# Optimization experiments

Hardware: AMD Instinct MI355X
Metric: run time of the kernel (lower is better)

## Reference

```python
import jax, jax.numpy as jnp
import numpy as np

N_NODES = 50000
N_EDGES = 800000
D_IN, D_HID, D_OUT = 16, 64, 16
N_BLOCKS = 4


def setup_inputs() -> dict:
    key = jax.random.key(0)
    ks = jax.random.split(key, 12)
    s = 0.05  # small init scale to keep sum-aggregation over 4 blocks stable
    return {
        "x": jax.random.normal(ks[0], (N_NODES, D_IN), jnp.float32),
        "lframes": jax.random.normal(ks[1], (N_NODES, 4, 4), jnp.float32),
        "edge_index": jax.random.randint(ks[2], (2, N_EDGES), 0, N_NODES, jnp.int64),
        "lin_in_w": jax.random.normal(ks[3], (D_IN, D_HID), jnp.float32) * s,
        "lin_in_b": jnp.zeros((D_HID,), jnp.float32),
        # per-block mlp1: Linear(2D->D), ReLU, Linear(D->D), ReLU, Linear(D->D)
        "w0": jax.random.normal(ks[4], (N_BLOCKS, 2 * D_HID, D_HID), jnp.float32) * s,
        "b0": jnp.zeros((N_BLOCKS, D_HID), jnp.float32),
        "w1": jax.random.normal(ks[5], (N_BLOCKS, D_HID, D_HID), jnp.float32) * s,
        "b1": jnp.zeros((N_BLOCKS, D_HID), jnp.float32),
        "w2": jax.random.normal(ks[6], (N_BLOCKS, D_HID, D_HID), jnp.float32) * s,
        "b2": jnp.zeros((N_BLOCKS, D_HID), jnp.float32),
        "lin_out_w": jax.random.normal(ks[7], (D_HID, D_OUT), jnp.float32) * s,
        "lin_out_b": jnp.zeros((D_OUT,), jnp.float32),
    }


def reference(x, lframes, edge_index, lin_in_w, lin_in_b,
              w0, b0, w1, b1, w2, b2, lin_out_w, lin_out_b):
    src = edge_index[0]  # x_j (source / neighbor)
    dst = edge_index[1]  # x_i (target / aggregation node)
    h = x @ lin_in_w + lin_in_b  # [N, D]
    for k in range(N_BLOCKS):
        # message: cat((x_j, x_i)) -> mlp1 ; mlp2 is Identity (num_layers_mlp2=0)
        m = jnp.concatenate((h[src], h[dst]), axis=-1)  # [E, 2D]
        m = jax.nn.relu(m @ w0[k] + b0[k])
        m = jax.nn.relu(m @ w1[k] + b1[k])
        m = m @ w2[k] + b2[k]  # [E, D]
        # aggregate: scatter-add at target node
        h = jax.ops.segment_sum(m, dst, num_segments=N_NODES)
    return h @ lin_out_w + lin_out_b  # [N, D_OUT]
```

## Files before the change

kernel.cpp:

```cpp
#include <hip/hip_runtime.h>
#include <hip/hip_bf16.h>

#define N_NODES 50000
#define N_EDGES 800000
#define D_IN    16
#define D_HID   64
#define D_OUT   16
#define NCHUNK  ((N_NODES + 255) / 256)
#define TMAX    100352
#define GE4     ((N_EDGES / 4 + 255) / 256)
#define GH      ((N_NODES * D_HID + 255) / 256)
#define SCAP    48
#define NSLOT4  (N_NODES * SCAP / 4)

typedef __hip_bfloat16 bf16;
typedef _Float16 f16;
typedef _Float16 f16x8 __attribute__((ext_vector_type(8)));
typedef float    f32x4 __attribute__((ext_vector_type(4)));
typedef _Float16 f16x8a __attribute__((ext_vector_type(8), may_alias));
typedef int      i32x4 __attribute__((ext_vector_type(4)));
typedef unsigned short u16x8a __attribute__((ext_vector_type(8), may_alias));
typedef float    f32x4a __attribute__((ext_vector_type(4), may_alias));

__device__ __forceinline__ float b2f(bf16 v) { return __bfloat162float(v); }
__device__ __forceinline__ float bfb(unsigned short u) {
    union { unsigned u; float f; } z; z.u = (unsigned)u << 16; return z.f;
}
__device__ __forceinline__ int clampn(int v) {
    return v < 0 ? 0 : (v >= N_NODES ? N_NODES - 1 : v);
}
__device__ __forceinline__ float rdf(const void* p, long i, int isbf) {
    return isbf ? b2f(((const bf16*)p)[i]) : ((const float*)p)[i];
}
__device__ __forceinline__ f16x8 relu8(f16x8 v) {
#pragma unroll
    for (int j = 0; j < 8; j++) v[j] = v[j] > (f16)0 ? v[j] : (f16)0;
    return v;
}
__device__ __forceinline__ int sbase(int m) {
    return (m & 0xFFFFF) * SCAP + ((m >> 25) & 3) * 16;
}

__global__ __launch_bounds__(256) void k_detect(const unsigned short* __restrict__ xw,
                                                const int* __restrict__ ei,
                                                int* __restrict__ flags,
                                                int* __restrict__ cursor,
                                                int* __restrict__ slots,
                                                unsigned short* __restrict__ psrc_us)
{
    int gtid = blockIdx.x * 256 + threadIdx.x;
    if (gtid < N_NODES) cursor[gtid] = 0;
    const i32x4 fillv = {N_NODES, N_NODES, N_NODES, N_NODES};
#pragma unroll
    for (int k = 0; k < 12; k++) {
        int q = k * (NCHUNK * 256) + gtid;
        if (q < NSLOT4) ((i32x4*)slots)[q] = fillv;
    }
    if (blockIdx.x == 0 && threadIdx.x < 64)
        psrc_us[(size_t)N_NODES * 64 + threadIdx.x] = 0xFC00u;
    if (blockIdx.x == 0 && threadIdx.x == 0) {
        int inband = 0;
        for (int j = 0; j < 256; j++) {
            unsigned short w = xw[2 * j];
            int e = (w >> 7) & 0xFF;
            if ((w & 0x7FFF) == 0 || (e >= 100 && e <= 140)) inband++;
        }
        flags[0] = (inband >= 192) ? 1 : 0;
        int z = 1;
        for (int j = 1; j < 128; j += 2) z &= (ei[j] == 0) ? 1 : 0;
        flags[1] = z;
    }
}

__global__ __launch_bounds__(256) void k_scatter4(const int* __restrict__ flags,
                                                  const int* __restrict__ eidx,
                                                  int* __restrict__ cursor,
                                                  int* __restrict__ slots)
{
    int base = (blockIdx.x * 256 + threadIdx.x) * 4;
    if (base >= N_EDGES) return;
    const int strd = flags[1] ? 2 : 1;
    const long dbase = flags[1] ? (long)(2 * N_EDGES) : (long)N_EDGES;
    int d[4], s[4], pos[4], cnt = min(4, N_EDGES - base);
#pragma unroll
    for (int j = 0; j < 4; j++)
        if (j < cnt) {
            d[j] = clampn(eidx[dbase + (long)(base + j) * strd]);
            s[j] = clampn(eidx[(long)(base + j) * strd]);
        }
#pragma unroll
    for (int j = 0; j < 4; j++)
        if (j < cnt) pos[j] = atomicAdd(&cursor[d[j]], 1);
#pragma unroll
    for (int j = 0; j < 4; j++)
        if (j < cnt && pos[j] < SCAP) slots[d[j] * SCAP + pos[j]] = s[j];
}

__global__ __launch_bounds__(256) void k_prep(const int* __restrict__ flags,
                                              const void* __restrict__ gw0,
                                              const void* __restrict__ gw1,
                                              const void* __restrict__ gw2,
                                              f16* __restrict__ wfrag,
                                              const void* __restrict__ x,
                                              const void* __restrict__ liw,
                                              const void* __restrict__ lib,
                                              float* __restrict__ h,
                                              const void* __restrict__ gb1,
                                              const void* __restrict__ gb2,
                                              float* __restrict__ cpad)
{
    const int isbf = flags[0];
    const int bid = blockIdx.x;
    if (bid < 32) {
        int idx = bid * 256 + threadIdx.x;
        int kb = idx >> 11, rem = idx & 2047;
        int slot = rem >> 6, lane = rem & 63;
        int lm = lane & 15, quad = lane >> 4;
        f16* outp = wfrag + (long)idx * 8;
        if (slot < 16) {
            int c = slot >> 2, q = slot & 3;
            long base = (long)kb * 2 * D_HID * D_HID;
#pragma unroll
            for (int j = 0; j < 8; j++)
                outp[j] = (f16)rdf(gw0, base + (long)(c * 32 + quad * 8 + j) * 64 + q * 16 + lm, isbf);
        } else {
            const void* gw = (slot < 24) ? gw1 : gw2;
            int s = (slot < 24) ? slot - 16 : slot - 24;
            int c = s >> 2, q = s & 3;
            long base = (long)kb * D_HID * D_HID;
#pragma unroll
            for (int j = 0; j < 8; j++)
                outp[j] = (f16)rdf(gw, base + (long)(c * 32 + quad * 8 + j) * 64 + q * 16 + lm, isbf);
        }
    } else if (bid < 32 + GH) {
        int idx = (bid - 32) * 256 + threadIdx.x;
        if (idx >= N_NODES * D_HID) return;
        int n = idx >> 6, c = idx & 63;
        float acc, wr[16], xr[16];
        if (isbf) {
            const unsigned short* xp = (const unsigned short*)x + (long)n * 16;
            u16x8a x0 = *(const u16x8a*)xp, x1 = *(const u16x8a*)(xp + 8);
#pragma unroll
            for (int i = 0; i < 8; i++) { xr[i] = bfb(x0[i]); xr[8 + i] = bfb(x1[i]); }
            const unsigned short* wq = (const unsigned short*)liw;
#pragma unroll
            for (int i = 0; i < 16; i++) wr[i] = bfb(wq[i * 64 + c]);
            acc = bfb(((const unsigned short*)lib)[c]);
        } else {
            const float* xp = (const float*)x + (long)n * 16;
#pragma unroll
            for (int q = 0; q < 4; q++) {
                f32x4a v = *(const f32x4a*)(xp + q * 4);
#pragma unroll
                for (int j = 0; j < 4; j++) xr[q * 4 + j] = v[j];
            }
            const float* wq = (const float*)liw;
#pragma unroll
            for (int i = 0; i < 16; i++) wr[i] = wq[i * 64 + c];
            acc = ((const float*)lib)[c];
        }
#pragma unroll
        for (int i = 0; i < 16; i++) acc += xr[i] * wr[i];
        h[idx] = acc;
    } else {
        int t = threadIdx.x;
        int k = t >> 6, j = t & 63;
        float acc = rdf(gb2, (long)k * 64 + j, isbf);
        for (int i = 0; i < 64; i++) {
            float zi = (float)(f16)fmaxf(rdf(gb1, (long)k * 64 + i, isbf), 0.f);
            float wi = (float)(f16)rdf(gw2, (long)k * 4096 + (long)i * 64 + j, isbf);
            acc += zi * wi;
        }
        cpad[k * 64 + j] = acc;
    }
}

__global__ __launch_bounds__(256) void k_scan1(const int* __restrict__ deg,
                                               int* __restrict__ bsum_t)
{
    __shared__ int rt[256];
    const int t = threadIdx.x;
    int i = blockIdx.x * 256 + t;
    int v = (i < N_NODES) ? deg[i] : 0;
    rt[t] = min((v + 15) >> 4, 3);
    __syncthreads();
    for (int d = 128; d > 0; d >>= 1) {
        if (t < d) rt[t] += rt[t + d];
        __syncthreads();
    }
    if (t == 0) bsum_t[blockIdx.x] = rt[0];
}

__global__ __launch_bounds__(256) void k_scan2(const int* __restrict__ bsum_t,
                                               int* __restrict__ boff_t,
                                               int* __restrict__ tot_t)
{
    __shared__ int st_[256];
    const int t = threadIdx.x;
    st_[t] = (t < NCHUNK) ? bsum_t[t] : 0;
    __syncthreads();
    for (int d = 1; d < 256; d <<= 1) {
        int vt = (t >= d) ? st_[t - d] : 0;
        __syncthreads();
        st_[t] += vt;
        __syncthreads();
    }
    if (t < NCHUNK) boff_t[t] = (t == 0) ? 0 : st_[t - 1];
    if (t == NCHUNK - 1) tot_t[0] = st_[t];
}

__global__ __launch_bounds__(256) void k_scan3(const int* __restrict__ deg,
                                               const int* __restrict__ boff_t,
                                               int* __restrict__ toff,
                                               int* __restrict__ tmeta)
{
    __shared__ int st_[256];
    const int t = threadIdx.x;
    int i = blockIdx.x * 256 + t;
    int v = (i < N_NODES) ? deg[i] : 0;
    int w = min((v + 15) >> 4, 3);
    st_[t] = w;
    __syncthreads();
    for (int d = 1; d < 256; d <<= 1) {
        int ut = (t >= d) ? st_[t - d] : 0;
        __syncthreads();
        st_[t] += ut;
        __syncthreads();
    }
    if (i < N_NODES) {
        int exT = boff_t[blockIdx.x] + st_[t] - w;
        toff[i] = exT;
        for (int j = 0; j < w; j++)
            tmeta[exT + j] = i | (min(16, v - 16 * j) << 20) | (j << 25);
    }
}

#define HP_ST 72

__global__ __launch_bounds__(256) void k_proj(
    const int* __restrict__ flags, float* hio,
    const f16* __restrict__ wfrag, const void* __restrict__ gb0,
    const int* __restrict__ deg,
    f16* __restrict__ psrc, f16* __restrict__ pdst, int kblk)
{
    __shared__ f16 hL_s[4][16 * HP_ST];

    const int tid  = threadIdx.x;
    const int isbf = flags[0];
    const int wv = tid >> 6, ln = tid & 63;
    const int lm = ln & 15, quad = ln >> 4;
    f16* hL = hL_s[wv];

    const int g = blockIdx.x * 4 + wv;
    if (g >= N_NODES / 16) return;
    const int n0 = g * 16;

    const f16* wb = wfrag + (long)kblk * 32 * 64 * 8;

#pragma unroll
    for (int i = 0; i < 16; i++) {
        int idx = i * 64 + ln;
        hL[(idx >> 6) * HP_ST + (idx & 63)] = (f16)hio[(long)n0 * 64 + idx];
    }
#pragma unroll
    for (int i = 0; i < 16; i++)
        if (deg[n0 + i] == 0) hio[(long)(n0 + i) * 64 + ln] = 0.f;

    f16x8 a[2];
#pragma unroll
    for (int c = 0; c < 2; c++)
        a[c] = *(const f16x8a*)&hL[lm * HP_ST + c * 32 + quad * 8];

    f32x4 accS[4], accD[4];
#pragma unroll
    for (int q = 0; q < 4; q++) {
        float bd = rdf(gb0, (long)kblk * 64 + q * 16 + lm, isbf);
        accS[q] = (f32x4){0.f, 0.f, 0.f, 0.f};
        accD[q] = (f32x4){bd, bd, bd, bd};
    }
#pragma unroll
    for (int c = 0; c < 2; c++)
#pragma unroll
        for (int q = 0; q < 4; q++) {
            f16x8 bs = *(const f16x8a*)&wb[(((c + 0) * 4 + q) * 64 + ln) * 8];
            f16x8 bd = *(const f16x8a*)&wb[(((c + 2) * 4 + q) * 64 + ln) * 8];
            accS[q] = __builtin_amdgcn_mfma_f32_16x16x32_f16(a[c], bs, accS[q], 0, 0, 0);
            accD[q] = __builtin_amdgcn_mfma_f32_16x16x32_f16(a[c], bd, accD[q], 0, 0, 0);
        }
#pragma unroll
    for (int q = 0; q < 4; q++)
#pragma unroll
        for (int r = 0; r < 4; r++) {
            long o = (long)(n0 + quad * 4 + r) * 64 + q * 16 + lm;
            psrc[o] = (f16)accS[q][r];
            pdst[o] = (f16)accD[q][r];
        }
}

#define Y_ST 72

__global__ __launch_bounds__(256) void k_edge_tile(
    const int* __restrict__ flags,
    const int* __restrict__ slots, const int* __restrict__ tmeta,
    const int* __restrict__ toff,
    const f16* __restrict__ psrc, const f16* __restrict__ pdst,
    float* __restrict__ hout,
    const f16* __restrict__ wfrag, const void* __restrict__ gb1,
    const void* __restrict__ gb2, const float* __restrict__ cpad, int kblk)
{
    __shared__ f16 y_s[4][16 * Y_ST];

    const int tid  = threadIdx.x;
    const int isbf = flags[0];
    const int wv = tid >> 6, ln = tid & 63;
    const int lm = ln & 15, quad = ln >> 4;
    const int sub = ln & 7, eh = ln >> 3;
    f16* y = y_s[wv];

    const f16* wb = wfrag + (long)kblk * 32 * 64 * 8;
    f16x8 bw1[2][4], bw2[2][4];
#pragma unroll
    for (int c = 0; c < 2; c++)
#pragma unroll
        for (int q = 0; q < 4; q++) {
            bw1[c][q] = *(const f16x8a*)&wb[((16 + c * 4 + q) * 64 + ln) * 8];
            bw2[c][q] = *(const f16x8a*)&wb[((24 + c * 4 + q) * 64 + ln) * 8];
        }
    float bias1[4], bias2[4], cp[4];
#pragma unroll
    for (int q = 0; q < 4; q++) {
        bias1[q] = rdf(gb1, (long)kblk * 64 + q * 16 + lm, isbf);
        bias2[q] = rdf(gb2, (long)kblk * 64 + q * 16 + lm, isbf);
        cp[q]    = cpad[kblk * 64 + q * 16 + lm];
    }

    const int T  = toff[N_NODES];
    const int W  = gridDim.x * 4;
    const int gw = blockIdx.x * 4 + wv;
    int t0 = (int)((long)gw * T / W);
    int t1 = (int)((long)(gw + 1) * T / W);
    if (t0 > 0)
        while (t0 < T && (tmeta[t0] & 0xFFFFF) == (tmeta[t0 - 1] & 0xFFFFF)) t0++;
    if (t1 > 0)
        while (t1 < T && (tmeta[t1] & 0xFFFFF) == (tmeta[t1 - 1] & 0xFFFFF)) t1++;
    if (t0 >= t1) return;

    int mA = tmeta[t0];
    int mB = tmeta[min(t0 + 1, T - 1)];
    int mC = tmeta[min(t0 + 2, T - 1)];
    int bA = sbase(mA), bB = sbase(mB);
    int sAa = slots[bA + eh], sAb = slots[bA + 8 + eh];
    int sBa = slots[bB + eh], sBb = slots[bB + 8 + eh];
    f16x8 psAa = *(const f16x8a*)&psrc[(long)sAa * 64 + sub * 8];
    f16x8 psAb = *(const f16x8a*)&psrc[(long)sAb * 64 + sub * 8];
    f16x8 pdA  = *(const f16x8a*)&pdst[(long)(mA & 0xFFFFF) * 64 + sub * 8];

    float accn[4] = {0.f, 0.f, 0.f, 0.f};

    for (int tt = t0; tt < t1; ++tt) {
        const int mD = tmeta[min(tt + 3, T - 1)];
        const int bC = sbase(mC);
        const int sCa = slots[bC + eh], sCb = slots[bC + 8 + eh];
        f16x8 psBa = *(const f16x8a*)&psrc[(long)sBa * 64 + sub * 8];
        f16x8 psBb = *(const f16x8a*)&psrc[(long)sBb * 64 + sub * 8];
        f16x8 pdB  = *(const f16x8a*)&pdst[(long)(mB & 0xFFFFF) * 64 + sub * 8];

        *(f16x8a*)&y[eh * Y_ST + sub * 8]       = relu8(psAa + pdA);
        *(f16x8a*)&y[(8 + eh) * Y_ST + sub * 8] = relu8(psAb + pdA);

        f16x8 a1[2];
        a1[0] = *(const f16x8a*)&y[lm * Y_ST + quad * 8];
        a1[1] = *(const f16x8a*)&y[lm * Y_ST + 32 + quad * 8];
        f32x4 acc[4];
#pragma unroll
        for (int q = 0; q < 4; q++)
            acc[q] = (f32x4){bias1[q], bias1[q], bias1[q], bias1[q]};
#pragma unroll
        for (int c = 0; c < 2; c++)
#pragma unroll
            for (int q = 0; q < 4; q++)
                acc[q] = __builtin_amdgcn_mfma_f32_16x16x32_f16(a1[c], bw1[c][q], acc[q], 0, 0, 0);
#pragma unroll
        for (int q = 0; q < 4; q++)
#pragma unroll
            for (int r = 0; r < 4; r++)
                y[(quad * 4 + r) * Y_ST + q * 16 + lm] = (f16)fmaxf(acc[q][r], 0.f);

        f16x8 a2[2];
        a2[0] = *(const f16x8a*)&y[lm * Y_ST + quad * 8];
        a2[1] = *(const f16x8a*)&y[lm * Y_ST + 32 + quad * 8];
#pragma unroll
        for (int q = 0; q < 4; q++)
            acc[q] = (f32x4){bias2[q], bias2[q], bias2[q], bias2[q]};
#pragma unroll
        for (int c = 0; c < 2; c++)
#pragma unroll
            for (int q = 0; q < 4; q++)
                acc[q] = __builtin_amdgcn_mfma_f32_16x16x32_f16(a2[c], bw2[c][q], acc[q], 0, 0, 0);

#pragma unroll
        for (int q = 0; q < 4; q++)
#pragma unroll
            for (int r = 0; r < 4; r++)
                accn[q] += acc[q][r];

        const int curn = mA & 0xFFFFF;
        const int nxt  = (tt + 1 < t1) ? (mB & 0xFFFFF) : -1;
        if (nxt != curn) {
            const float npad = (float)(16 - ((mA >> 20) & 31));
#pragma unroll
            for (int q = 0; q < 4; q++) {
                float v = accn[q];
                v += __shfl_xor(v, 16, 64);
                v += __shfl_xor(v, 32, 64);
                if (quad == 0) hout[(long)curn * 64 + q * 16 + lm] = v - npad * cp[q];
                accn[q] = 0.f;
            }
        }

        mA = mB; mB = mC; mC = mD;
        sBa = sCa; sBb = sCb;
        psAa = psBa; psAb = psBb; pdA = pdB;
    }
}

__global__ __launch_bounds__(256) void k_lin_out(const int* __restrict__ flags,
                                                 const float* __restrict__ h,
                                                 const void* __restrict__ w,
                                                 const void* __restrict__ b,
                                                 float* __restrict__ out)
{
    int idx = blockIdx.x * 256 + threadIdx.x;
    if (idx >= N_NODES * D_OUT) return;
    const int isbf = flags[0];
    int n = idx >> 4, c = idx & 15;
    float acc = rdf(b, c, isbf);
    const float* hr = h + (long)n * D_HID;
#pragma unroll
    for (int i = 0; i < D_HID; i++) acc += hr[i] * rdf(w, (long)i * D_OUT + c, isbf);
    out[idx] = acc;
}

extern "C" void kernel_launch(void* const* d_in, const int* in_sizes, int n_in,
                              void* d_out, int out_size, void* d_ws, size_t ws_size,
                              hipStream_t stream)
{
    const void* x    = d_in[0];
    const int*  ei   = (const int*)d_in[2];
    const void* liw  = d_in[3];
    const void* lib  = d_in[4];
    const void* w0   = d_in[5];
    const void* b0   = d_in[6];
    const void* w1   = d_in[7];
    const void* b1   = d_in[8];
    const void* w2   = d_in[9];
    const void* b2   = d_in[10];
    const void* low  = d_in[11];
    const void* lob  = d_in[12];
    float* out = (float*)d_out;

    char* wp = (char*)d_ws;
    int*   flags  = (int*)wp;                 wp += 256;
    float* hA     = (float*)wp;               wp += (size_t)N_NODES * D_HID * 4;
    f16*   Psrc   = (f16*)wp;                 wp += ((size_t)N_NODES + 1) * D_HID * 2;
    f16*   Pdst   = (f16*)wp;                 wp += (size_t)N_NODES * D_HID * 2;
    f16*   wfrag  = (f16*)wp;                 wp += (size_t)4 * 32 * 64 * 8 * 2;
    float* cpad   = (float*)wp;               wp += (size_t)4 * 64 * 4;
    int*   cursor = (int*)wp;                 wp += (size_t)N_NODES * 4;
    int*   bsum_t = (int*)wp;                 wp += 256 * 4;
    int*   boff_t = (int*)wp;                 wp += 256 * 4;
    int*   tmeta  = (int*)wp;                 wp += (size_t)TMAX * 4;
    int*   slots  = (int*)wp;                 wp += (size_t)N_NODES * SCAP * 4;
    int*   toff   = (int*)wp;

    k_detect<<<NCHUNK, 256, 0, stream>>>((const unsigned short*)x, ei, flags,
                                         cursor, slots, (unsigned short*)Psrc);
    k_scatter4<<<GE4, 256, 0, stream>>>(flags, ei, cursor, slots);
    k_prep<<<32 + GH + 1, 256, 0, stream>>>(flags, w0, w1, w2, wfrag,
                                            x, liw, lib, hA, b1, b2, cpad);

    k_scan1<<<NCHUNK, 256, 0, stream>>>(cursor, bsum_t);
    k_scan2<<<1, 256, 0, stream>>>(bsum_t, boff_t, toff + N_NODES);
    k_scan3<<<NCHUNK, 256, 0, stream>>>(cursor, boff_t, toff, tmeta);

    for (int k = 0; k < 4; k++) {
        k_proj<<<(N_NODES / 16 + 3) / 4, 256, 0, stream>>>(flags, hA, wfrag, b0,
                                                           cursor, Psrc, Pdst, k);
        k_edge_tile<<<1024, 256, 0, stream>>>(flags, slots, tmeta, toff,
                                              Psrc, Pdst, hA, wfrag, b1, b2,
                                              cpad, k);
    }

    k_lin_out<<<(N_NODES * D_OUT + 255) / 256, 256, 0, stream>>>(flags, hA, low, lob, out);
}
```

Baseline: 435.2 us.

## Store neighbor slots as 16-bit indices, widen scatter, cache lin_out weights in LDS

Shrinks the per-node neighbor slot array from 32-bit to 16-bit source indices, which halves slot fill and read traffic. The fill pattern becomes 0xC350 (50000) in each half-word. The scatter kernel now handles 8 edges per thread, k_lin_out stages weights and bias in shared memory and reads h with vector loads, and the edge tile kernel launches twice as many blocks. 16-bit indices only work because N_NODES fits in an unsigned short; the hidden edge kernel code must read slots as u16 correctly.

```diff
diff --git a/kernel.cpp b/kernel.cpp
--- a/kernel.cpp
+++ b/kernel.cpp
@@ -8,10 +8,10 @@
 #define D_OUT   16
 #define NCHUNK  ((N_NODES + 255) / 256)
 #define TMAX    100352
-#define GE4     ((N_EDGES / 4 + 255) / 256)
+#define GE8     ((N_EDGES / 8 + 255) / 256)
 #define GH      ((N_NODES * D_HID + 255) / 256)
 #define SCAP    48
-#define NSLOT4  (N_NODES * SCAP / 4)
+#define NSLOTV  (N_NODES * SCAP / 8)
 
 typedef __hip_bfloat16 bf16;
 typedef _Float16 f16;
@@ -45,16 +45,17 @@
                                                 const int* __restrict__ ei,
                                                 int* __restrict__ flags,
                                                 int* __restrict__ cursor,
-                                                int* __restrict__ slots,
+                                                unsigned short* __restrict__ slots,
                                                 unsigned short* __restrict__ psrc_us)
 {
     int gtid = blockIdx.x * 256 + threadIdx.x;
     if (gtid < N_NODES) cursor[gtid] = 0;
-    const i32x4 fillv = {N_NODES, N_NODES, N_NODES, N_NODES};
-#pragma unroll
-    for (int k = 0; k < 12; k++) {
+    const int dpat = (int)0xC350C350;
+    const i32x4 fillv = {dpat, dpat, dpat, dpat};
+#pragma unroll
+    for (int k = 0; k < 6; k++) {
         int q = k * (NCHUNK * 256) + gtid;
-        if (q < NSLOT4) ((i32x4*)slots)[q] = fillv;
+        if (q < NSLOTV) ((i32x4*)slots)[q] = fillv;
     }
     if (blockIdx.x == 0 && threadIdx.x < 64)
         psrc_us[(size_t)N_NODES * 64 + threadIdx.x] = 0xFC00u;
@@ -72,28 +73,29 @@
     }
 }
 
-__global__ __launch_bounds__(256) void k_scatter4(const int* __restrict__ flags,
+__global__ __launch_bounds__(256) void k_scatter8(const int* __restrict__ flags,
                                                   const int* __restrict__ eidx,
                                                   int* __restrict__ cursor,
-                                                  int* __restrict__ slots)
-{
-    int base = (blockIdx.x * 256 + threadIdx.x) * 4;
+                                                  unsigned short* __restrict__ slots)
+{
+    int base = (blockIdx.x * 256 + threadIdx.x) * 8;
     if (base >= N_EDGES) return;
     const int strd = flags[1] ? 2 : 1;
     const long dbase = flags[1] ? (long)(2 * N_EDGES) : (long)N_EDGES;
-    int d[4], s[4], pos[4], cnt = min(4, N_EDGES - base);
-#pragma unroll
-    for (int j = 0; j < 4; j++)
+    int d[8], s[8], pos[8], cnt = min(8, N_EDGES - base);
+#pragma unroll
+    for (int j = 0; j < 8; j++)
         if (j < cnt) {
             d[j] = clampn(eidx[dbase + (long)(base + j) * strd]);
             s[j] = clampn(eidx[(long)(base + j) * strd]);
         }
 #pragma unroll
-    for (int j = 0; j < 4; j++)
+    for (int j = 0; j < 8; j++)
         if (j < cnt) pos[j] = atomicAdd(&cursor[d[j]], 1);
 #pragma unroll
-    for (int j = 0; j < 4; j++)
-        if (j < cnt && pos[j] < SCAP) slots[d[j] * SCAP + pos[j]] = s[j];
+    for (int j = 0; j < 8; j++)
+        if (j < cnt && pos[j] < SCAP)
+            slots[d[j] * SCAP + pos[j]] = (unsigned short)s[j];
 }
 
 __global__ __launch_bounds__(256) void k_prep(const int* __restrict__ flags,
@@ -301,7 +303,7 @@
 
 __global__ __launch_bounds__(256) void k_edge_tile(
     const int* __restrict__ flags,
-    const int* __restrict__ slots, const int* __restrict__ tmeta,
+    const unsigned short* __restrict__ slots, const int* __restrict__ tmeta,
     const int* __restrict__ toff,
     const f16* __restrict__ psrc, const f16* __restrict__ pdst,
     float* __restrict__ hout,
@@ -430,14 +432,25 @@
                                                  const void* __restrict__ b,
                                                  float* __restrict__ out)
 {
-    int idx = blockIdx.x * 256 + threadIdx.x;
+    __shared__ float wl[D_HID * D_OUT];
+    __shared__ float bl[D_OUT];
+    const int isbf = flags[0];
+    const int t = threadIdx.x;
+    for (int k = t; k < D_HID * D_OUT; k += 256) wl[k] = rdf(w, k, isbf);
+    if (t < D_OUT) bl[t] = rdf(b, t, isbf);
+    __syncthreads();
+
+    int idx = blockIdx.x * 256 + t;
     if (idx >= N_NODES * D_OUT) return;
-    const int isbf = flags[0];
     int n = idx >> 4, c = idx & 15;
-    float acc = rdf(b, c, isbf);
     const float* hr = h + (long)n * D_HID;
-#pragma unroll
-    for (int i = 0; i < D_HID; i++) acc += hr[i] * rdf(w, (long)i * D_OUT + c, isbf);
+    float acc = bl[c];
+#pragma unroll
+    for (int i = 0; i < 16; i++) {
+        f32x4a v = *(const f32x4a*)(hr + i * 4);
+        acc += v[0] * wl[(i * 4 + 0) * 16 + c] + v[1] * wl[(i * 4 + 1) * 16 + c]
+             + v[2] * wl[(i * 4 + 2) * 16 + c] + v[3] * wl[(i * 4 + 3) * 16 + c];
+    }
     out[idx] = acc;
 }
 
@@ -470,12 +483,12 @@
     int*   bsum_t = (int*)wp;                 wp += 256 * 4;
     int*   boff_t = (int*)wp;                 wp += 256 * 4;
     int*   tmeta  = (int*)wp;                 wp += (size_t)TMAX * 4;
-    int*   slots  = (int*)wp;                 wp += (size_t)N_NODES * SCAP * 4;
+    unsigned short* slots = (unsigned short*)wp; wp += (size_t)N_NODES * SCAP * 2;
     int*   toff   = (int*)wp;
 
     k_detect<<<NCHUNK, 256, 0, stream>>>((const unsigned short*)x, ei, flags,
                                          cursor, slots, (unsigned short*)Psrc);
-    k_scatter4<<<GE4, 256, 0, stream>>>(flags, ei, cursor, slots);
+    k_scatter8<<<GE8, 256, 0, stream>>>(flags, ei, cursor, slots);
     k_prep<<<32 + GH + 1, 256, 0, stream>>>(flags, w0, w1, w2, wfrag,
                                             x, liw, lib, hA, b1, b2, cpad);
 
@@ -486,7 +499,7 @@
     for (int k = 0; k < 4; k++) {
         k_proj<<<(N_NODES / 16 + 3) / 4, 256, 0, stream>>>(flags, hA, wfrag, b0,
                                                            cursor, Psrc, Pdst, k);
-        k_edge_tile<<<1024, 256, 0, stream>>>(flags, slots, tmeta, toff,
+        k_edge_tile<<<2048, 256, 0, stream>>>(flags, slots, tmeta, toff,
                                               Psrc, Pdst, hA, wfrag, b1, b2,
                                               cpad, k);
     }
```

New measurement: 414.7 us. 4.7% less time.
